# Kernel optimization log

Measured on AMD Instinct MI355X. Metric: run time of the kernel, lower is better.

The kernel has to match this reference:

```python
import jax, jax.numpy as jnp
import numpy as np
import math
from itertools import permutations

B, C_IN, C_OUT, K, N, D, F_DIM = 2, 4, 8, 4, 224, 2, 128


def _make_perms(k):
    # [k!, k, k] permutation matrices, same ordering as itertools.permutations
    nP = math.factorial(k)
    perms = np.zeros((nP, k, k), dtype=np.float32)
    for c, p in enumerate(permutations(range(k))):
        perms[c, np.arange(k), np.array(p)] = 1.0
    return jnp.asarray(perms)


def setup_inputs() -> dict:
    key = jax.random.key(0)
    ks = jax.random.split(key, 6)
    graph = jax.random.normal(ks[0], (B, C_IN, N, N), jnp.float32)
    types = jax.random.normal(ks[1], (B, C_IN, N), jnp.float32)
    features = jax.random.normal(ks[2], (B, N, F_DIM), jnp.float32)
    # xavier-uniform-ish scales for the learned kernels
    k_struct = jax.random.normal(ks[3], (C_OUT, C_IN, K, K), jnp.float32) * 0.3
    k_row = jax.random.normal(ks[4], (C_OUT, C_IN, K), jnp.float32) * 0.5
    k_col = jax.random.normal(ks[5], (C_OUT, C_IN, K), jnp.float32) * 0.5
    return {"graph": graph, "types": types, "features": features,
            "k_struct": k_struct, "k_row": k_row, "k_col": k_col}


def _forward(graph, types, features, k_struct, k_row, k_col):
    Bn, C, Nn, _ = graph.shape
    k = k_struct.shape[-1]
    new_k = (k - 1) * D + 1
    nH = Nn - new_k + 1            # square graph -> nW == nH
    n_sub = nH * nH
    idx = jnp.arange(nH)[:, None] + jnp.arange(k) * D  # [nH, k] dilated window indices

    # --- _prepare: dilated subgraph extraction (vectorized gather) ---
    g = graph[:, :, idx, :]            # [B,C,nH,k,N]
    g = g[..., idx]                    # [B,C,nH,k,nH,k]
    sub = jnp.transpose(g, (0, 2, 4, 1, 3, 5)).reshape(Bn, n_sub, C, k, k)
    rt = jnp.transpose(types[:, :, idx], (0, 2, 1, 3))  # [B,nH,C,k]
    row_t = jnp.broadcast_to(rt[:, :, None], (Bn, nH, nH, C, k)).reshape(Bn, n_sub, C, k)
    col_t = jnp.broadcast_to(rt[:, None, :], (Bn, nH, nH, C, k)).reshape(Bn, n_sub, C, k)
    rf = features[:, idx, :].sum(axis=-2)              # [B,nH,F]
    feats = rf[:, :, None, :] + rf[:, None, :, :]      # row_features + col_features
    h_mean = feats.reshape(Bn, n_sub, -1).mean(axis=1)  # [B,F]

    # --- permuted kernels ---
    perms = _make_perms(k)                                  # [P,k,k]
    Kp = jnp.einsum('pau,oiuv,pbv->oipab', perms, k_struct, perms)  # P K P^T
    Rp = jnp.einsum('pau,oiu->oipa', perms, k_row)
    Cp = jnp.einsum('pau,oiu->oipa', perms, k_col)

    subf = sub.reshape(-1, C, k, k)   # [n,i,a,b], n = B*n_sub
    rtf = row_t.reshape(-1, C, k)
    ctf = col_t.reshape(-1, C, k)

    # ||X - Y||_F^2 = ||X||^2 + ||Y||^2 - 2<X,Y>, avoids the huge broadcasted diff
    def sq_dist(x2_ni, y2_opi, cross_nopi):
        return y2_opi[None] + x2_ni[:, None, None, :] - 2.0 * cross_nopi

    G2 = jnp.sum(subf * subf, axis=(-2, -1))                       # [n,i]
    K2 = jnp.transpose(jnp.sum(Kp * Kp, axis=(-2, -1)), (0, 2, 1))  # [o,p,i]
    struct = sq_dist(G2, K2, jnp.einsum('niab,oipab->nopi', subf, Kp))
    R2 = jnp.transpose(jnp.sum(Rp * Rp, axis=-1), (0, 2, 1))
    rsim = sq_dist(jnp.sum(rtf * rtf, axis=-1), R2, jnp.einsum('nia,oipa->nopi', rtf, Rp))
    C2 = jnp.transpose(jnp.sum(Cp * Cp, axis=-1), (0, 2, 1))
    csim = sq_dist(jnp.sum(ctf * ctf, axis=-1), C2, jnp.einsum('nia,oipa->nopi', ctf, Cp))

    total = struct + rsim + csim            # [n, o, P, i]
    # maxpool over P of (-total), negated back == min over permutations of total
    pooled = jnp.min(total, axis=2)         # [n, o, i]
    sims = jnp.transpose(pooled.reshape(Bn, n_sub, -1), (0, 2, 1))  # [B, o*i, n_sub]
    out_sim = (1.0 - jax.nn.softmax(sims, axis=-1)) / sims.shape[-1]
    return h_mean, out_sim


def reference(graph, types, features, k_struct, k_row, k_col):
    return _forward(graph, types, features, k_struct, k_row, k_col)
```

## Files before the change

### kernel.cpp

```cpp
#include <hip/hip_runtime.h>
#include <hip/hip_bf16.h>

#define B_    2
#define CIN   4
#define COUT  8
#define KK    4
#define DD    2
#define NN    224
#define FDIM  128
#define NH    218
#define NSUB  (NH*NH)
#define NPERM 24
#define NROWS (B_*COUT*CIN)
#define NSUB4 (NSUB/4)
#define CH4   512
#define MB    ((NSUB4 + CH4 - 1) / CH4)
#define OG    2
#define NCH2  ((NSUB + 511) / 512)
#define NW    4
#define NEGBIG (-3.4e38f)

typedef float v2f __attribute__((ext_vector_type(2)));

__device__ static constexpr int PERM[NPERM][4] = {
  {0,1,2,3},{0,1,3,2},{0,2,1,3},{0,2,3,1},{0,3,1,2},{0,3,2,1},
  {1,0,2,3},{1,0,3,2},{1,2,0,3},{1,2,3,0},{1,3,0,2},{1,3,2,0},
  {2,0,1,3},{2,0,3,1},{2,1,0,3},{2,1,3,0},{2,3,0,1},{2,3,1,0},
  {3,0,1,2},{3,0,2,1},{3,1,0,2},{3,1,2,0},{3,2,0,1},{3,2,1,0}
};

__global__ __launch_bounds__(64) void hmean_kernel(const float* __restrict__ features,
                                                   float* __restrict__ out) {
  int bf = blockIdx.x;
  int b = bf / FDIM, f = bf - b * FDIM;
  int lane = threadIdx.x;
  const float* fb = features + (size_t)b * NN * FDIM + f;
  float acc = 0.f;
  for (int r = lane; r < NN; r += 64) {
    int w = 0;
#pragma unroll
    for (int a = 0; a < KK; ++a) {
      int i0 = r - a * DD;
      if (0 <= i0 && i0 < NH) w++;
    }
    acc += (float)w * fb[(size_t)r * FDIM];
  }
#pragma unroll
  for (int off = 32; off > 0; off >>= 1) acc += __shfl_down(acc, off, 64);
  if (lane == 0) out[bf] = acc * (2.0f / (float)NH);
}

__global__ __launch_bounds__(256) void sims_kernel(
    const float* __restrict__ graph, const float* __restrict__ types,
    const float* __restrict__ ksA, const float* __restrict__ krA,
    const float* __restrict__ kcA, float* __restrict__ simsOut,
    float* __restrict__ partial)
{
  __shared__ float ls[COUT * CIN * 16];
  __shared__ float lr[COUT * CIN * 4];
  __shared__ float lc[COUT * CIN * 4];
  __shared__ float lK2[COUT * CIN];
  int t = threadIdx.x;
  for (int i = t; i < COUT * CIN * 16; i += 256) ls[i] = ksA[i];
  for (int i = t; i < COUT * CIN * 4; i += 256) { lr[i] = krA[i]; lc[i] = kcA[i]; }
  __syncthreads();
  if (t < COUT * CIN) {
    float k2 = 0.f;
#pragma unroll
    for (int u = 0; u < 16; ++u) k2 += ls[t * 16 + u] * ls[t * 16 + u];
#pragma unroll
    for (int u = 0; u < 4; ++u) k2 += lr[t * 4 + u] * lr[t * 4 + u] + lc[t * 4 + u] * lc[t * 4 + u];
    lK2[t] = k2;
  }
  __syncthreads();

  int s0r = blockIdx.x * 512 + t;
  int s1r = s0r + 256;
  bool v0 = (s0r < NSUB), v1 = (s1r < NSUB);
  int s0 = v0 ? s0r : (NSUB - 1);
  int s1 = v1 ? s1r : (NSUB - 1);
  int yi  = blockIdx.y;
  int og  = yi >> 3;
  int bci = yi & 7;
  int b   = bci >> 2;
  int ci  = bci & 3;
  int ii0 = s0 / NH, jj0 = s0 - ii0 * NH;
  int ii1 = s1 / NH, jj1 = s1 - ii1 * NH;

  const float* gi = graph + ((size_t)b * CIN + ci) * NN * NN;
  const float* ti = types + ((size_t)b * CIN + ci) * NN;

  v2f subv[16], rtv[4], ctv[4];
  v2f G2 = 0.f, T2r = 0.f, T2c = 0.f;
#pragma unroll
  for (int a = 0; a < KK; ++a) {
    const float* r0 = gi + (size_t)(ii0 + a * DD) * NN + jj0;
    const float* r1 = gi + (size_t)(ii1 + a * DD) * NN + jj1;
#pragma unroll
    for (int bb = 0; bb < KK; ++bb) {
      v2f v; v.x = r0[bb * DD]; v.y = r1[bb * DD];
      subv[a * 4 + bb] = v;
      G2 += v * v;
    }
    v2f rv; rv.x = ti[ii0 + a * DD]; rv.y = ti[ii1 + a * DD];
    v2f cv; cv.x = ti[jj0 + a * DD]; cv.y = ti[jj1 + a * DD];
    rtv[a] = rv; ctv[a] = cv;
    T2r += rv * rv; T2c += cv * cv;
  }
  v2f base0 = G2 + T2r + T2c;

  int wave = t >> 6, lane = t & 63;

#pragma unroll 1
  for (int oo = 0; oo < COUT / OG; ++oo) {
    int o = og * (COUT / OG) + oo;
    int oc = o * CIN + ci;
    float kS[16], kR[4], kC[4];
    {
      const float4* pS4 = (const float4*)(ls + oc * 16);
#pragma unroll
      for (int u = 0; u < 4; ++u) {
        float4 q = pS4[u];
        kS[u*4+0] = q.x; kS[u*4+1] = q.y; kS[u*4+2] = q.z; kS[u*4+3] = q.w;
      }
      float4 qr = *(const float4*)(lr + oc * 4);
      kR[0] = qr.x; kR[1] = qr.y; kR[2] = qr.z; kR[3] = qr.w;
      float4 qc = *(const float4*)(lc + oc * 4);
      kC[0] = qc.x; kC[1] = qc.y; kC[2] = qc.z; kC[3] = qc.w;
    }

    v2f C1[16];
#pragma unroll
    for (int a = 0; a < 4; ++a)
#pragma unroll
      for (int ap = 0; ap < 4; ++ap)
        C1[a * 4 + ap] = subv[a * 4 + a] * kS[ap * 4 + ap]
                       + rtv[a] * kR[ap] + ctv[a] * kC[ap];

    v2f maxcr = NEGBIG;
#pragma unroll
    for (int p = 0; p < NPERM; ++p) {
      const int p0 = PERM[p][0], p1 = PERM[p][1], p2 = PERM[p][2], p3 = PERM[p][3];
      v2f cr = C1[0 * 4 + p0] + C1[1 * 4 + p1] + C1[2 * 4 + p2] + C1[3 * 4 + p3];
      cr += subv[0*4+1] * kS[p0*4+p1];
      cr += subv[0*4+2] * kS[p0*4+p2];
      cr += subv[0*4+3] * kS[p0*4+p3];
      cr += subv[1*4+0] * kS[p1*4+p0];
      cr += subv[1*4+2] * kS[p1*4+p2];
      cr += subv[1*4+3] * kS[p1*4+p3];
      cr += subv[2*4+0] * kS[p2*4+p0];
      cr += subv[2*4+1] * kS[p2*4+p1];
      cr += subv[2*4+3] * kS[p2*4+p3];
      cr += subv[3*4+0] * kS[p3*4+p0];
      cr += subv[3*4+1] * kS[p3*4+p1];
      cr += subv[3*4+2] * kS[p3*4+p2];
      maxcr = __builtin_elementwise_max(maxcr, cr);
    }
    v2f best = base0 + lK2[oc] - 2.0f * maxcr;

    int rowIdx = (b * COUT + o) * CIN + ci;
    size_t rowbase = (size_t)rowIdx * NSUB;
    if (v0) simsOut[rowbase + s0r] = best.x;
    if (v1) simsOut[rowbase + s1r] = best.y;

    float bm0 = v0 ? best.x : NEGBIG;
    float bm1 = v1 ? best.y : NEGBIG;
    float m = fmaxf(bm0, bm1);
#pragma unroll
    for (int off = 32; off > 0; off >>= 1) m = fmaxf(m, __shfl_down(m, off, 64));
    m = __shfl(m, 0, 64);
    float e = 0.f;
    if (v0) e += __expf(bm0 - m);
    if (v1) e += __expf(bm1 - m);
#pragma unroll
    for (int off = 32; off > 0; off >>= 1) e += __shfl_down(e, off, 64);
    if (lane == 0) {
      int idx = ((rowIdx * NCH2 + blockIdx.x) * NW + wave) * 2;
      partial[idx] = m; partial[idx + 1] = e;
    }
  }
}

__global__ __launch_bounds__(256) void softmax_combine(const float* __restrict__ partial,
                                                       float* __restrict__ stats) {
  int row = blockIdx.x;
  int t = threadIdx.x;
  const float* pp = partial + (size_t)row * NCH2 * NW * 2;
  float m = NEGBIG, l = 0.f;
  for (int i = t; i < NCH2 * NW; i += 256) {
    float mi = pp[2 * i], li = pp[2 * i + 1];
    float M = fmaxf(m, mi);
    l = l * __expf(m - M) + li * __expf(mi - M);
    m = M;
  }
  __shared__ float ms[256], lsv[256];
  ms[t] = m; lsv[t] = l;
  __syncthreads();
  for (int off = 128; off > 0; off >>= 1) {
    if (t < off) {
      float m2 = ms[t + off], l2 = lsv[t + off];
      float M = fmaxf(ms[t], m2);
      lsv[t] = lsv[t] * __expf(ms[t] - M) + l2 * __expf(m2 - M);
      ms[t] = M;
    }
    __syncthreads();
  }
  if (t == 0) { stats[2 * row] = ms[0]; stats[2 * row + 1] = 1.0f / lsv[0]; }
}

__global__ __launch_bounds__(256) void softmax_final(float* __restrict__ sims,
                                                     const float* __restrict__ stats) {
  int blk = blockIdx.x;
  int row = blk / MB;
  int ch  = blk - row * MB;
  int base4 = ch * CH4;
  int n4 = NSUB4 - base4; if (n4 > CH4) n4 = CH4;
  float4* rp = (float4*)(sims + (size_t)row * NSUB) + base4;
  float M = stats[2 * row], invS = stats[2 * row + 1];
  const float scale = 1.0f / (float)NSUB;
  for (int i = threadIdx.x; i < n4; i += 256) {
    float4 v = rp[i];
    v.x = (1.0f - __expf(v.x - M) * invS) * scale;
    v.y = (1.0f - __expf(v.y - M) * invS) * scale;
    v.z = (1.0f - __expf(v.z - M) * invS) * scale;
    v.w = (1.0f - __expf(v.w - M) * invS) * scale;
    rp[i] = v;
  }
}

extern "C" void kernel_launch(void* const* d_in, const int* in_sizes, int n_in,
                              void* d_out, int out_size, void* d_ws, size_t ws_size,
                              hipStream_t stream) {
  const float* graph    = (const float*)d_in[0];
  const float* types    = (const float*)d_in[1];
  const float* features = (const float*)d_in[2];
  const float* ks       = (const float*)d_in[3];
  const float* kr       = (const float*)d_in[4];
  const float* kc       = (const float*)d_in[5];
  float* out  = (float*)d_out;
  float* sims = out + B_ * FDIM;

  float* partial = (float*)d_ws;
  float* stats   = partial + NROWS * NCH2 * NW * 2;

  hmean_kernel<<<B_ * FDIM, 64, 0, stream>>>(features, out);
  dim3 sgrid(NCH2, B_ * CIN * OG);
  sims_kernel<<<sgrid, 256, 0, stream>>>(graph, types, ks, kr, kc, sims, partial);
  softmax_combine<<<NROWS, 256, 0, stream>>>(partial, stats);
  softmax_final<<<NROWS * MB, 256, 0, stream>>>(sims, stats);
}
```

Measured before the change: 108.2 us.

## Precompute pairwise permutation partial sums and fuse softmax combine into final pass

The inner permutation loop now reuses precomputed pair sums for positions (0,1) and (2,3), which cuts the per-permutation multiply-adds from 12 cross terms plus 4 adds to 8 cross terms plus 1 add. The separate softmax_combine kernel is removed. Every softmax_final block now redundantly reduces that row's partial (max, sum) entries itself before normalising its chunk. This saves one kernel launch and a global round trip, but repeats the row reduction in every block and adds register pressure from the 24 pair values.

```diff
diff --git a/kernel.cpp b/kernel.cpp
--- a/kernel.cpp
+++ b/kernel.cpp
@@ -18,6 +18,7 @@
 #define OG    2
 #define NCH2  ((NSUB + 511) / 512)
 #define NW    4
+#define NPART (NCH2*NW)
 #define NEGBIG (-3.4e38f)
 
 typedef float v2f __attribute__((ext_vector_type(2)));
@@ -137,23 +138,31 @@
         C1[a * 4 + ap] = subv[a * 4 + a] * kS[ap * 4 + ap]
                        + rtv[a] * kR[ap] + ctv[a] * kC[ap];
 
+    v2f pair01[16], pair23[16];
+#pragma unroll
+    for (int x = 0; x < 4; ++x)
+#pragma unroll
+      for (int y = 0; y < 4; ++y) {
+        if (x == y) continue;
+        pair01[x * 4 + y] = C1[0 * 4 + x] + C1[1 * 4 + y]
+                          + subv[0*4+1] * kS[x*4+y] + subv[1*4+0] * kS[y*4+x];
+        pair23[x * 4 + y] = C1[2 * 4 + x] + C1[3 * 4 + y]
+                          + subv[2*4+3] * kS[x*4+y] + subv[3*4+2] * kS[y*4+x];
+      }
+
     v2f maxcr = NEGBIG;
 #pragma unroll
     for (int p = 0; p < NPERM; ++p) {
       const int p0 = PERM[p][0], p1 = PERM[p][1], p2 = PERM[p][2], p3 = PERM[p][3];
-      v2f cr = C1[0 * 4 + p0] + C1[1 * 4 + p1] + C1[2 * 4 + p2] + C1[3 * 4 + p3];
-      cr += subv[0*4+1] * kS[p0*4+p1];
+      v2f cr = pair01[p0 * 4 + p1] + pair23[p2 * 4 + p3];
       cr += subv[0*4+2] * kS[p0*4+p2];
+      cr += subv[2*4+0] * kS[p2*4+p0];
       cr += subv[0*4+3] * kS[p0*4+p3];
-      cr += subv[1*4+0] * kS[p1*4+p0];
+      cr += subv[3*4+0] * kS[p3*4+p0];
       cr += subv[1*4+2] * kS[p1*4+p2];
+      cr += subv[2*4+1] * kS[p2*4+p1];
       cr += subv[1*4+3] * kS[p1*4+p3];
-      cr += subv[2*4+0] * kS[p2*4+p0];
-      cr += subv[2*4+1] * kS[p2*4+p1];
-      cr += subv[2*4+3] * kS[p2*4+p3];
-      cr += subv[3*4+0] * kS[p3*4+p0];
       cr += subv[3*4+1] * kS[p3*4+p1];
-      cr += subv[3*4+2] * kS[p3*4+p2];
       maxcr = __builtin_elementwise_max(maxcr, cr);
     }
     v2f best = base0 + lK2[oc] - 2.0f * maxcr;
@@ -181,13 +190,16 @@
   }
 }
 
-__global__ __launch_bounds__(256) void softmax_combine(const float* __restrict__ partial,
-                                                       float* __restrict__ stats) {
-  int row = blockIdx.x;
+__global__ __launch_bounds__(256) void softmax_final(float* __restrict__ sims,
+                                                     const float* __restrict__ partial) {
+  int blk = blockIdx.x;
+  int row = blk / MB;
+  int ch  = blk - row * MB;
   int t = threadIdx.x;
-  const float* pp = partial + (size_t)row * NCH2 * NW * 2;
+
+  const float* pp = partial + (size_t)row * NPART * 2;
   float m = NEGBIG, l = 0.f;
-  for (int i = t; i < NCH2 * NW; i += 256) {
+  for (int i = t; i < NPART; i += 256) {
     float mi = pp[2 * i], li = pp[2 * i + 1];
     float M = fmaxf(m, mi);
     l = l * __expf(m - M) + li * __expf(mi - M);
@@ -205,20 +217,13 @@
     }
     __syncthreads();
   }
-  if (t == 0) { stats[2 * row] = ms[0]; stats[2 * row + 1] = 1.0f / lsv[0]; }
-}
-
-__global__ __launch_bounds__(256) void softmax_final(float* __restrict__ sims,
-                                                     const float* __restrict__ stats) {
-  int blk = blockIdx.x;
-  int row = blk / MB;
-  int ch  = blk - row * MB;
+  float M = ms[0], invS = 1.0f / lsv[0];
+
   int base4 = ch * CH4;
   int n4 = NSUB4 - base4; if (n4 > CH4) n4 = CH4;
   float4* rp = (float4*)(sims + (size_t)row * NSUB) + base4;
-  float M = stats[2 * row], invS = stats[2 * row + 1];
   const float scale = 1.0f / (float)NSUB;
-  for (int i = threadIdx.x; i < n4; i += 256) {
+  for (int i = t; i < n4; i += 256) {
     float4 v = rp[i];
     v.x = (1.0f - __expf(v.x - M) * invS) * scale;
     v.y = (1.0f - __expf(v.y - M) * invS) * scale;
@@ -241,11 +246,9 @@
   float* sims = out + B_ * FDIM;
 
   float* partial = (float*)d_ws;
-  float* stats   = partial + NROWS * NCH2 * NW * 2;
 
   hmean_kernel<<<B_ * FDIM, 64, 0, stream>>>(features, out);
   dim3 sgrid(NCH2, B_ * CIN * OG);
   sims_kernel<<<sgrid, 256, 0, stream>>>(graph, types, ks, kr, kc, sims, partial);
-  softmax_combine<<<NROWS, 256, 0, stream>>>(partial, stats);
-  softmax_final<<<NROWS * MB, 256, 0, stream>>>(sims, stats);
-}
+  softmax_final<<<NROWS * MB, 256, 0, stream>>>(sims, partial);
+}
```

Measured after the change: 103.7 us. 4.2% less time.
